# Optimization experiments

Hardware: AMD Instinct MI355X
Metric: run time of the kernel (lower is better)

Reference implementation:

```python
import jax, jax.numpy as jnp
import numpy as np

B, S, D, H = 2, 2048, 1024, 16
DH = D // H

def setup_inputs() -> dict:
    key = jax.random.key(0)
    ks = jax.random.split(key, 12)
    def lin(kw, kb, fan_in):
        bound = 1.0 / np.sqrt(fan_in)
        W = jax.random.uniform(kw, (D, D), jnp.float32, -bound, bound)
        b = jax.random.uniform(kb, (D,), jnp.float32, -bound, bound)
        return W, b
    Wq, bq = lin(ks[0], ks[1], D)
    Wk, bk = lin(ks[2], ks[3], D)
    Wv, bv = lin(ks[4], ks[5], D)
    Wo, bo = lin(ks[6], ks[7], D)
    q = jax.random.normal(ks[8], (B, S, D), jnp.float32)
    k = jax.random.normal(ks[9], (B, S, D), jnp.float32)
    v = jax.random.normal(ks[10], (B, S, D), jnp.float32)
    # causal mask (1 = keep, 0 = masked), broadcastable to [B,H,S,S]
    mask = jnp.tril(jnp.ones((S, S), jnp.int32))[None, None, :, :]
    return {"q": q, "k": k, "v": v, "mask": mask,
            "Wq": Wq, "bq": bq, "Wk": Wk, "bk": bk,
            "Wv": Wv, "bv": bv, "Wo": Wo, "bo": bo}

def reference(q, k, v, mask, Wq, bq, Wk, bk, Wv, bv, Wo, bo):
    # projections: torch Linear is x @ W.T + b
    def split(x):  # [B,S,D] -> [B,H,S,DH]
        return x.reshape(B, S, H, DH).transpose(0, 2, 1, 3)
    qh = split(q @ Wq.T + bq)
    kh = split(k @ Wk.T + bk)
    vh = split(v @ Wv.T + bv)
    score = jnp.einsum('bhqd,bhkd->bhqk', qh, kh) / jnp.sqrt(jnp.float32(DH))
    score = jnp.where(mask == 0, jnp.float32(-1e9), score)
    attn = jax.nn.softmax(score, axis=-1)
    out = jnp.einsum('bhqk,bhkd->bhqd', attn, vh)
    out = out.transpose(0, 2, 1, 3).reshape(B, S, D)
    return out @ Wo.T + bo, attn
```

## Files before the change

### kernel.cpp

```cpp
#include <hip/hip_runtime.h>

#define S_LEN 2048
#define D_MODEL 1024
#define N_HEADS 16
#define D_HEAD 64
#define BATCH 2

typedef __bf16 bf16;
typedef __bf16 bf16x8 __attribute__((ext_vector_type(8)));
typedef __bf16 bf16x4 __attribute__((ext_vector_type(4)));
typedef float f32x4 __attribute__((ext_vector_type(4)));

__device__ __forceinline__ f32x4 mfma16(bf16x8 a, bf16x8 b, f32x4 c) {
  return __builtin_amdgcn_mfma_f32_16x16x32_bf16(a, b, c, 0, 0, 0);
}

__device__ __forceinline__ void gload16(const bf16* g, bf16* lds) {
  __builtin_amdgcn_global_load_lds((const __attribute__((address_space(1))) void*)g,
                                   (__attribute__((address_space(3))) void*)lds, 16, 0, 0);
}

__global__ __launch_bounds__(256) void cvt_w(
    const float* __restrict__ s0, const float* __restrict__ s1,
    const float* __restrict__ s2, const float* __restrict__ s3,
    bf16* __restrict__ d0, bf16* __restrict__ d1, bf16* __restrict__ d2,
    bf16* __restrict__ d3) {
  const int y = blockIdx.y;
  const float* s = (y == 0) ? s0 : (y == 1) ? s1 : (y == 2) ? s2 : s3;
  bf16* d = (y == 0) ? d0 : (y == 1) ? d1 : (y == 2) ? d2 : d3;
  const int i = blockIdx.x * blockDim.x + threadIdx.x;
  const f32x4 a = *(const f32x4*)(s + (size_t)i * 8);
  const f32x4 b = *(const f32x4*)(s + (size_t)i * 8 + 4);
  bf16x8 o;
  o[0] = (bf16)a[0]; o[1] = (bf16)a[1]; o[2] = (bf16)a[2]; o[3] = (bf16)a[3];
  o[4] = (bf16)b[0]; o[5] = (bf16)b[1]; o[6] = (bf16)b[2]; o[7] = (bf16)b[3];
  *(bf16x8*)(d + (size_t)i * 8) = o;
}

__device__ __forceinline__ void gemm_loop(const bf16* __restrict__ gA,
                                          const bf16* __restrict__ gB,
                                          bf16* As, bf16* Bs,
                                          f32x4 (&acc)[4][4], int tid) {
  const int l = tid & 63;
  const int w = tid >> 6;
  const int wr = w >> 1, wc = w & 1;
  const int lr = l & 15, lg = l >> 4;
  const int lrow8 = l >> 3;
  const int colg = ((l & 7) ^ (lrow8 & 7)) * 8;

  for (int k0 = 0; k0 < D_MODEL; k0 += 64) {
#pragma unroll
    for (int i = 0; i < 4; ++i) {
      const int c = w * 4 + i;
      const int row = c * 8 + lrow8;
      gload16(gA + (size_t)row * D_MODEL + k0 + colg, As + c * 512);
      gload16(gB + (size_t)row * D_MODEL + k0 + colg, Bs + c * 512);
    }
    __syncthreads();
#pragma unroll
    for (int half = 0; half < 2; ++half) {
      bf16x8 af[4], bfb[4];
#pragma unroll
      for (int mm = 0; mm < 4; ++mm) {
        const int row = wr * 64 + mm * 16 + lr;
        af[mm] = *(const bf16x8*)(As + row * 64 + ((half * 4 + lg) ^ (lr & 7)) * 8);
      }
#pragma unroll
      for (int nn = 0; nn < 4; ++nn) {
        const int row = wc * 64 + nn * 16 + lr;
        bfb[nn] = *(const bf16x8*)(Bs + row * 64 + ((half * 4 + lg) ^ (lr & 7)) * 8);
      }
#pragma unroll
      for (int mm = 0; mm < 4; ++mm)
#pragma unroll
        for (int nn = 0; nn < 4; ++nn)
          acc[mm][nn] = mfma16(af[mm], bfb[nn], acc[mm][nn]);
    }
    __syncthreads();
  }
}

__device__ __forceinline__ void gemm_loop_af32(const float* __restrict__ gA32,
                                               const bf16* __restrict__ gB,
                                               bf16* As, bf16* Bs,
                                               f32x4 (&acc)[4][4], int tid) {
  const int l = tid & 63;
  const int w = tid >> 6;
  const int wr = w >> 1, wc = w & 1;
  const int lr = l & 15, lg = l >> 4;
  const int lrow8 = l >> 3;
  const int colg = ((l & 7) ^ (lrow8 & 7)) * 8;

  const int arow = tid >> 1;
  const int ahalf = tid & 1;
  const float* aptr = gA32 + (size_t)arow * D_MODEL + ahalf * 32;
  bf16* awr = As + arow * 64;

  for (int k0 = 0; k0 < D_MODEL; k0 += 64) {
    f32x4 av[8];
#pragma unroll
    for (int c = 0; c < 8; ++c) av[c] = *(const f32x4*)(aptr + k0 + c * 4);
#pragma unroll
    for (int i = 0; i < 4; ++i) {
      const int c = w * 4 + i;
      const int row = c * 8 + lrow8;
      gload16(gB + (size_t)row * D_MODEL + k0 + colg, Bs + c * 512);
    }
#pragma unroll
    for (int c8 = 0; c8 < 4; ++c8) {
      bf16x8 o;
#pragma unroll
      for (int e = 0; e < 4; ++e) {
        o[e] = (bf16)av[c8 * 2][e];
        o[e + 4] = (bf16)av[c8 * 2 + 1][e];
      }
      const int col16 = ahalf * 4 + c8;
      *(bf16x8*)(awr + (col16 ^ (arow & 7)) * 8) = o;
    }
    __syncthreads();
#pragma unroll
    for (int half = 0; half < 2; ++half) {
      bf16x8 af[4], bfb[4];
#pragma unroll
      for (int mm = 0; mm < 4; ++mm) {
        const int row = wr * 64 + mm * 16 + lr;
        af[mm] = *(const bf16x8*)(As + row * 64 + ((half * 4 + lg) ^ (lr & 7)) * 8);
      }
#pragma unroll
      for (int nn = 0; nn < 4; ++nn) {
        const int row = wc * 64 + nn * 16 + lr;
        bfb[nn] = *(const bf16x8*)(Bs + row * 64 + ((half * 4 + lg) ^ (lr & 7)) * 8);
      }
#pragma unroll
      for (int mm = 0; mm < 4; ++mm)
#pragma unroll
        for (int nn = 0; nn < 4; ++nn)
          acc[mm][nn] = mfma16(af[mm], bfb[nn], acc[mm][nn]);
    }
    __syncthreads();
  }
}

__global__ __launch_bounds__(256) void gemm_qkv(
    const float* __restrict__ qf, const float* __restrict__ kf,
    const float* __restrict__ vf, const bf16* __restrict__ Wqb,
    const bf16* __restrict__ Wkb, const bf16* __restrict__ Wvb,
    const float* __restrict__ biasq, const float* __restrict__ biask,
    const float* __restrict__ biasv, bf16* __restrict__ qhw,
    bf16* __restrict__ khw, bf16* __restrict__ vtw) {
  __shared__ bf16 As[128 * 64];
  __shared__ bf16 Bs[128 * 64];
  __shared__ bf16 T[128][72];
  const int z = blockIdx.z;
  const float* A = (z == 0) ? qf : (z == 1) ? kf : vf;
  const bf16* W = (z == 0) ? Wqb : (z == 1) ? Wkb : Wvb;
  const float* bias = (z == 0) ? biasq : (z == 1) ? biask : biasv;
  const float scale = (z == 0) ? 0.125f : 1.0f;
  bf16* out = (z == 0) ? qhw : (z == 1) ? khw : vtw;

  const int tid = threadIdx.x;
  const int l = tid & 63;
  const int w = tid >> 6;
  const int wr = w >> 1, wc = w & 1;
  const int lr = l & 15, lg = l >> 4;

  f32x4 acc[4][4] = {};
  gemm_loop_af32(A + ((size_t)blockIdx.x * 128) * D_MODEL,
                 W + ((size_t)blockIdx.y * 128) * D_MODEL, As, Bs, acc, tid);

  const int b = (blockIdx.x * 128) >> 11;
  const int s0 = (blockIdx.x * 128) & 2047;

  if (z == 2) {
#pragma unroll
    for (int half = 0; half < 2; ++half) {
      if (wc == half) {
#pragma unroll
        for (int nn = 0; nn < 4; ++nn) {
          const int n = blockIdx.y * 128 + half * 64 + nn * 16 + lr;
          const float bv = bias[n];
#pragma unroll
          for (int mm = 0; mm < 4; ++mm)
#pragma unroll
            for (int r = 0; r < 4; ++r) {
              const int ml = wr * 64 + mm * 16 + lg * 4 + r;
              T[ml][nn * 16 + lr] = (bf16)(acc[mm][nn][r] + bv);
            }
        }
      }
      __syncthreads();
      const int d = tid & 63;
      const int sblk = (tid >> 6) * 32;
      const int hglob = blockIdx.y * 2 + half;
      bf16* orow = vtw + (((size_t)(b * N_HEADS + hglob)) * D_HEAD + d) * S_LEN + s0 + sblk;
#pragma unroll
      for (int j = 0; j < 4; ++j) {
        bf16x8 pk;
#pragma unroll
        for (int e = 0; e < 8; ++e) pk[e] = T[sblk + j * 8 + e][d];
        *(bf16x8*)(orow + j * 8) = pk;
      }
      __syncthreads();
    }
  } else {
#pragma unroll
    for (int half = 0; half < 2; ++half) {
      if (wc == half) {
#pragma unroll
        for (int nn = 0; nn < 4; ++nn) {
          const int n = blockIdx.y * 128 + half * 64 + nn * 16 + lr;
          const float bv = bias[n];
#pragma unroll
          for (int mm = 0; mm < 4; ++mm)
#pragma unroll
            for (int r = 0; r < 4; ++r) {
              const int ml = wr * 64 + mm * 16 + lg * 4 + r;
              T[ml][nn * 16 + lr] = (bf16)((acc[mm][nn][r] + bv) * scale);
            }
        }
      }
      __syncthreads();
      const int hglob = blockIdx.y * 2 + half;
      bf16* obase = out + ((size_t)(b * N_HEADS + hglob) * S_LEN + s0) * D_HEAD;
      const int rsub = tid >> 3;
      const int d8 = (tid & 7) * 8;
#pragma unroll
      for (int j = 0; j < 4; ++j) {
        const int row_l = j * 32 + rsub;
        *(bf16x8*)(obase + (size_t)row_l * D_HEAD + d8) = *(const bf16x8*)(&T[row_l][d8]);
      }
      __syncthreads();
    }
  }
}

__device__ __forceinline__ void stage_strip(const bf16* __restrict__ src,
                                            size_t rstride, bf16* lds, int tid) {
#pragma unroll
  for (int rnd = 0; rnd < 2; ++rnd) {
    const int chunk = rnd * 256 + tid;
    const int row = chunk >> 3;
    const int c8 = chunk & 7;
    const int src8 = c8 ^ (row & 7);
    gload16(src + (size_t)row * rstride + src8 * 8, lds + chunk * 8);
  }
}

__global__ __launch_bounds__(256) void attn_flash(const bf16* __restrict__ qh,
                                                  const bf16* __restrict__ kh,
                                                  const bf16* __restrict__ vt,
                                                  bf16* __restrict__ ctx,
                                                  float* __restrict__ lbuf) {
  __shared__ bf16 Kb[2][64 * 64];
  __shared__ bf16 Vb[2][64 * 64];
  __shared__ bf16 P[4][16][72];
  const int tid = threadIdx.x;
  const int w = tid >> 6, l = tid & 63;
  const int lr = l & 15, lg = l >> 4;
  const int bh = blockIdx.y;
  const int bxx = blockIdx.x;
  const int qgroup = (bxx & 1) ? (31 - (bxx >> 1)) : (bxx >> 1);
  const int q0 = qgroup * 64 + w * 16;
  const int qrow = q0 + lr;
  const bf16* qp = qh + (size_t)bh * S_LEN * D_HEAD;
  const bf16* kp = kh + (size_t)bh * S_LEN * D_HEAD;
  const bf16* vp = vt + (size_t)bh * D_HEAD * S_LEN;

  const bf16x8 qf0 = *(const bf16x8*)(qp + (size_t)qrow * D_HEAD + lg * 8);
  const bf16x8 qf1 = *(const bf16x8*)(qp + (size_t)qrow * D_HEAD + 32 + lg * 8);

  const float NINF = -__builtin_inff();
  const int nfull = qgroup;
  const int x0 = (lg ^ (lr & 7)) * 8;
  const int x1 = ((4 | lg) ^ (lr & 7)) * 8;

  stage_strip(kp, D_HEAD, Kb[0], tid);
  stage_strip(vp, S_LEN, Vb[0], tid);
  __syncthreads();

  float lsum = 0.f;
  f32x4 oacc[4] = {};
  int cur = 0;

  for (int st = 0; st < nfull; ++st) {
    stage_strip(kp + (size_t)(st + 1) * 64 * D_HEAD, D_HEAD, Kb[cur ^ 1], tid);
    stage_strip(vp + (st + 1) * 64, S_LEN, Vb[cur ^ 1], tid);

    float ps = 0.f;
    __builtin_amdgcn_s_setprio(1);
    f32x4 zz4[4];
#pragma unroll
    for (int t = 0; t < 4; ++t) {
      const bf16* krow = Kb[cur] + (t * 16 + lr) * 64;
      f32x4 zz = {};
      zz = mfma16(*(const bf16x8*)(krow + x0), qf0, zz);
      zz = mfma16(*(const bf16x8*)(krow + x1), qf1, zz);
      zz4[t] = zz;
    }
    __builtin_amdgcn_s_setprio(0);
#pragma unroll
    for (int t = 0; t < 4; ++t) {
      bf16x4 pk;
#pragma unroll
      for (int r = 0; r < 4; ++r) {
        const float e = __expf(fminf(zz4[t][r], 60.f));
        ps += e;
        pk[r] = (bf16)e;
      }
      *(bf16x4*)(&P[w][lr][t * 16 + lg * 4]) = pk;
    }
    ps += __shfl_xor(ps, 16);
    ps += __shfl_xor(ps, 32);
    lsum += ps;
    const bf16x8 pb0 = *(const bf16x8*)(&P[w][lr][lg * 8]);
    const bf16x8 pb1 = *(const bf16x8*)(&P[w][lr][32 + lg * 8]);
    __builtin_amdgcn_s_setprio(1);
#pragma unroll
    for (int dt = 0; dt < 4; ++dt) {
      const bf16* vrow = Vb[cur] + (dt * 16 + lr) * 64;
      oacc[dt] = mfma16(*(const bf16x8*)(vrow + x0), pb0, oacc[dt]);
      oacc[dt] = mfma16(*(const bf16x8*)(vrow + x1), pb1, oacc[dt]);
    }
    __builtin_amdgcn_s_setprio(0);
    __syncthreads();
    cur ^= 1;
  }

  {
    float ps = 0.f;
#pragma unroll
    for (int t = 0; t < 4; ++t) {
      bf16x4 pk;
      if (t <= w) {
        const bf16* krow = Kb[cur] + (t * 16 + lr) * 64;
        f32x4 zz = {};
        zz = mfma16(*(const bf16x8*)(krow + x0), qf0, zz);
        zz = mfma16(*(const bf16x8*)(krow + x1), qf1, zz);
#pragma unroll
        for (int r = 0; r < 4; ++r) {
          const float sv = (t == w && (lg * 4 + r) > lr) ? NINF : zz[r];
          const float e = __expf(fminf(sv, 60.f));
          ps += e;
          pk[r] = (bf16)e;
        }
      } else {
#pragma unroll
        for (int r = 0; r < 4; ++r) pk[r] = (bf16)0.f;
      }
      *(bf16x4*)(&P[w][lr][t * 16 + lg * 4]) = pk;
    }
    ps += __shfl_xor(ps, 16);
    ps += __shfl_xor(ps, 32);
    lsum += ps;
    const bf16x8 pb0 = *(const bf16x8*)(&P[w][lr][lg * 8]);
    const bf16x8 pb1 = *(const bf16x8*)(&P[w][lr][32 + lg * 8]);
#pragma unroll
    for (int dt = 0; dt < 4; ++dt) {
      const bf16* vrow = Vb[cur] + (dt * 16 + lr) * 64;
      oacc[dt] = mfma16(*(const bf16x8*)(vrow + x0), pb0, oacc[dt]);
      oacc[dt] = mfma16(*(const bf16x8*)(vrow + x1), pb1, oacc[dt]);
    }
  }

  const float invl = 1.0f / lsum;
  const int b = bh >> 4, h = bh & 15;
  bf16* crow = ctx + ((size_t)(b * S_LEN + qrow)) * D_MODEL + h * D_HEAD;
#pragma unroll
  for (int dt = 0; dt < 4; ++dt) {
    bf16x4 ov;
#pragma unroll
    for (int r = 0; r < 4; ++r) ov[r] = (bf16)(oacc[dt][r] * invl);
    *(bf16x4*)(crow + dt * 16 + lg * 4) = ov;
  }
  if (lg == 0) lbuf[(size_t)bh * S_LEN + qrow] = invl;
}

__global__ __launch_bounds__(256) void mat_out(
    const bf16* __restrict__ qh, const bf16* __restrict__ kh,
    const float* __restrict__ lbuf, float* __restrict__ attn,
    const bf16* __restrict__ ctxA, const bf16* __restrict__ Wo,
    const float* __restrict__ bo, float* __restrict__ outp) {
  __shared__ __align__(16) char smem[34048];
  const int bid = blockIdx.x;
  const int tid = threadIdx.x;
  const int w = tid >> 6, l = tid & 63;
  const int lr = l & 15, lg = l >> 4;

  if (bid < 256) {
    bf16* As = (bf16*)smem;
    bf16* Bs = (bf16*)(smem + 16384);
    const int bx = bid & 31, by = bid >> 5;
    const int wr = w >> 1, wc = w & 1;
    f32x4 acc[4][4] = {};
    gemm_loop(ctxA + ((size_t)bx * 128) * D_MODEL,
              Wo + ((size_t)by * 128) * D_MODEL, As, Bs, acc, tid);
    const int rowg0 = bx * 128 + wr * 64;
    const int colg0 = by * 128 + wc * 64;
#pragma unroll
    for (int nn = 0; nn < 4; ++nn) {
      const int n = colg0 + nn * 16 + lr;
      const float bv = bo[n];
#pragma unroll
      for (int mm = 0; mm < 4; ++mm)
#pragma unroll
        for (int r = 0; r < 4; ++r) {
          const int m = rowg0 + mm * 16 + lg * 4 + r;
          __builtin_nontemporal_store(acc[mm][nn][r] + bv,
                                      outp + (size_t)m * D_MODEL + n);
        }
    }
    return;
  }

  bf16* Pt = (bf16*)smem;
  const int mid = bid - 256;
  const int q0 = (mid & 31) * 64;
  const int k0b = ((mid >> 5) & 7) * 256;
  const int bh = mid >> 8;
  float* ap = attn + (size_t)bh * S_LEN * S_LEN;

  if (k0b > q0 + 63) {
    const f32x4 zv = {};
#pragma unroll
    for (int j = 0; j < 4; ++j) {
      const int q = q0 + w * 16 + j * 4 + lg;
      float* rp = ap + (size_t)q * S_LEN + k0b + lr * 4;
#pragma unroll
      for (int sub = 0; sub < 4; ++sub)
        __builtin_nontemporal_store(zv, (f32x4*)(rp + sub * 64));
    }
    return;
  }

  const int k0 = k0b + w * 64;
  if (k0 <= q0 + 63) {
    const bf16* qp = qh + (size_t)bh * S_LEN * D_HEAD;
    const bf16* kp = kh + (size_t)bh * S_LEN * D_HEAD;
    float iv[4];
#pragma unroll
    for (int qs = 0; qs < 4; ++qs)
      iv[qs] = lbuf[(size_t)bh * S_LEN + q0 + qs * 16 + lr];
    bf16x8 kf[4][2], qf[4][2];
#pragma unroll
    for (int kt = 0; kt < 4; ++kt) {
      kf[kt][0] = *(const bf16x8*)(kp + (size_t)(k0 + kt * 16 + lr) * D_HEAD + lg * 8);
      kf[kt][1] = *(const bf16x8*)(kp + (size_t)(k0 + kt * 16 + lr) * D_HEAD + 32 + lg * 8);
    }
#pragma unroll
    for (int qs = 0; qs < 4; ++qs) {
      qf[qs][0] = *(const bf16x8*)(qp + (size_t)(q0 + qs * 16 + lr) * D_HEAD + lg * 8);
      qf[qs][1] = *(const bf16x8*)(qp + (size_t)(q0 + qs * 16 + lr) * D_HEAD + 32 + lg * 8);
    }
    f32x4 acc[4][4] = {};
#pragma unroll
    for (int qs = 0; qs < 4; ++qs)
#pragma unroll
      for (int kt = 0; kt < 4; ++kt) {
        acc[qs][kt] = mfma16(kf[kt][0], qf[qs][0], acc[qs][kt]);
        acc[qs][kt] = mfma16(kf[kt][1], qf[qs][1], acc[qs][kt]);
      }
#pragma unroll
    for (int qs = 0; qs < 4; ++qs) {
      const int q = q0 + qs * 16 + lr;
#pragma unroll
      for (int kt = 0; kt < 4; ++kt) {
        const int kbase = k0 + kt * 16 + lg * 4;
        bf16x4 pk;
#pragma unroll
        for (int r = 0; r < 4; ++r) {
          const float pv = (kbase + r > q)
                               ? 0.f
                               : __expf(fminf(acc[qs][kt][r], 60.f)) * iv[qs];
          pk[r] = (bf16)pv;
        }
        *(bf16x4*)(Pt + (qs * 16 + lr) * 264 + w * 64 + kt * 16 + lg * 4) = pk;
      }
    }
  } else {
    const bf16x4 z4 = {};
#pragma unroll
    for (int j = 0; j < 16; ++j)
      *(bf16x4*)(Pt + (j * 4 + lg) * 264 + w * 64 + lr * 4) = z4;
  }
  __syncthreads();

#pragma unroll
  for (int j = 0; j < 4; ++j) {
    const int rowl = w * 16 + j * 4 + lg;
    float* rp = ap + (size_t)(q0 + rowl) * S_LEN + k0b + lr * 4;
#pragma unroll
    for (int sub = 0; sub < 4; ++sub) {
      const bf16x4 pk = *(const bf16x4*)(Pt + rowl * 264 + sub * 64 + lr * 4);
      f32x4 o;
      o[0] = (float)pk[0]; o[1] = (float)pk[1];
      o[2] = (float)pk[2]; o[3] = (float)pk[3];
      __builtin_nontemporal_store(o, (f32x4*)(rp + sub * 64));
    }
  }
}

extern "C" void kernel_launch(void* const* d_in, const int* in_sizes, int n_in,
                              void* d_out, int out_size, void* d_ws, size_t ws_size,
                              hipStream_t stream) {
  (void)in_sizes; (void)n_in; (void)out_size; (void)ws_size;
  const float* q  = (const float*)d_in[0];
  const float* k  = (const float*)d_in[1];
  const float* v  = (const float*)d_in[2];
  const float* Wq = (const float*)d_in[4];
  const float* bq = (const float*)d_in[5];
  const float* Wk = (const float*)d_in[6];
  const float* bk = (const float*)d_in[7];
  const float* Wv = (const float*)d_in[8];
  const float* bv = (const float*)d_in[9];
  const float* Wo = (const float*)d_in[10];
  const float* bo = (const float*)d_in[11];

  float* outp = (float*)d_out;
  float* attn = outp + (size_t)BATCH * S_LEN * D_MODEL;

  char* ws = (char*)d_ws;
  bf16* qhw  = (bf16*)(ws);
  bf16* khw  = (bf16*)(ws + (8u << 20));
  bf16* vtw  = (bf16*)(ws + (16u << 20));
  bf16* ctxb = (bf16*)(ws + (24u << 20));
  bf16* Wqb  = (bf16*)(ws + (32u << 20));
  bf16* Wkb  = (bf16*)(ws + (34u << 20));
  bf16* Wvb  = (bf16*)(ws + (36u << 20));
  bf16* Wob  = (bf16*)(ws + (38u << 20));
  float* lbuf = (float*)(ws + (40u << 20));

  dim3 bb(256);
  cvt_w<<<dim3(512, 4), bb, 0, stream>>>(Wq, Wk, Wv, Wo, Wqb, Wkb, Wvb, Wob);
  gemm_qkv<<<dim3(32, 8, 3), bb, 0, stream>>>(q, k, v, Wqb, Wkb, Wvb,
                                              bq, bk, bv, qhw, khw, vtw);
  attn_flash<<<dim3(32, 32), bb, 0, stream>>>(qhw, khw, vtw, ctxb, lbuf);
  mat_out<<<dim3(8448), bb, 0, stream>>>(qhw, khw, lbuf, attn,
                                         ctxb, Wob, bo, outp);
}
```

Measured before the change: 277.0 us.

## Widen attention q-tile to 128 rows and move masked-zero attn stores into flash kernel

Each attention wave now processes two 16-row query fragments, so every K/V fragment read from LDS feeds twice as many MFMAs. Blocks cover 128 query rows, and the diagonal tile is handled inside the main loop per wave. Zero-filling of the fully masked upper-triangle attention blocks moves from mat_out into extra blocks of attn_flash, so the zero stores overlap with flash compute. mat_out then launches only the lower-triangular tiles, indexed through a triangular decode. This adds register pressure and some causal load imbalance across waves.

Result: slower. 286.7 us (+3.5%).

```diff
diff --git a/kernel.cpp b/kernel.cpp
--- a/kernel.cpp
+++ b/kernel.cpp
@@ -246,133 +246,184 @@
   }
 }
 
-__global__ __launch_bounds__(256) void attn_flash(const bf16* __restrict__ qh,
-                                                  const bf16* __restrict__ kh,
-                                                  const bf16* __restrict__ vt,
-                                                  bf16* __restrict__ ctx,
-                                                  float* __restrict__ lbuf) {
-  __shared__ bf16 Kb[2][64 * 64];
-  __shared__ bf16 Vb[2][64 * 64];
-  __shared__ bf16 P[4][16][72];
+__global__ __launch_bounds__(256) void attn_flash(
+    const bf16* __restrict__ qh, const bf16* __restrict__ kh,
+    const bf16* __restrict__ vt, bf16* __restrict__ ctx,
+    float* __restrict__ lbuf, float* __restrict__ attn) {
+  __shared__ bf16 Kb[2][4096];
+  __shared__ bf16 Vb[2][4096];
+  __shared__ bf16 P[4][2][16][72];
   const int tid = threadIdx.x;
   const int w = tid >> 6, l = tid & 63;
   const int lr = l & 15, lg = l >> 4;
-  const int bh = blockIdx.y;
-  const int bxx = blockIdx.x;
-  const int qgroup = (bxx & 1) ? (31 - (bxx >> 1)) : (bxx >> 1);
-  const int q0 = qgroup * 64 + w * 16;
-  const int qrow = q0 + lr;
+  const int bx = blockIdx.x, bh = blockIdx.y;
+
+  if (bx >= 16) {
+    int rem = bx - 16, zq = 0, cnt = 7;
+    while (rem >= cnt) { rem -= cnt; --cnt; ++zq; }
+    const int kq = zq + 1 + rem;
+    float* base = attn + (size_t)bh * S_LEN * S_LEN + (size_t)(zq * 256) * S_LEN + kq * 256;
+    const f32x4 zv = {};
+    for (int it = 0; it < 64; ++it) {
+      float* rp = base + (size_t)(it * 4 + w) * S_LEN + l * 4;
+      __builtin_nontemporal_store(zv, (f32x4*)rp);
+    }
+    return;
+  }
+
+  const int qg = (bx & 1) ? (15 - (bx >> 1)) : (bx >> 1);
+  const int q0w = qg * 128 + w * 32;
   const bf16* qp = qh + (size_t)bh * S_LEN * D_HEAD;
   const bf16* kp = kh + (size_t)bh * S_LEN * D_HEAD;
   const bf16* vp = vt + (size_t)bh * D_HEAD * S_LEN;
 
-  const bf16x8 qf0 = *(const bf16x8*)(qp + (size_t)qrow * D_HEAD + lg * 8);
-  const bf16x8 qf1 = *(const bf16x8*)(qp + (size_t)qrow * D_HEAD + 32 + lg * 8);
+  bf16x8 qf[2][2];
+#pragma unroll
+  for (int f = 0; f < 2; ++f) {
+    qf[f][0] = *(const bf16x8*)(qp + (size_t)(q0w + f * 16 + lr) * D_HEAD + lg * 8);
+    qf[f][1] = *(const bf16x8*)(qp + (size_t)(q0w + f * 16 + lr) * D_HEAD + 32 + lg * 8);
+  }
 
   const float NINF = -__builtin_inff();
-  const int nfull = qgroup;
   const int x0 = (lg ^ (lr & 7)) * 8;
   const int x1 = ((4 | lg) ^ (lr & 7)) * 8;
+  const int nfull = 2 * qg + (w >> 1);
+  const int smax = 2 * qg + 1;
 
   stage_strip(kp, D_HEAD, Kb[0], tid);
   stage_strip(vp, S_LEN, Vb[0], tid);
   __syncthreads();
 
-  float lsum = 0.f;
-  f32x4 oacc[4] = {};
+  float lsum[2] = {0.f, 0.f};
+  f32x4 oacc[2][4] = {};
   int cur = 0;
 
-  for (int st = 0; st < nfull; ++st) {
-    stage_strip(kp + (size_t)(st + 1) * 64 * D_HEAD, D_HEAD, Kb[cur ^ 1], tid);
-    stage_strip(vp + (st + 1) * 64, S_LEN, Vb[cur ^ 1], tid);
-
-    float ps = 0.f;
-    __builtin_amdgcn_s_setprio(1);
-    f32x4 zz4[4];
-#pragma unroll
-    for (int t = 0; t < 4; ++t) {
-      const bf16* krow = Kb[cur] + (t * 16 + lr) * 64;
-      f32x4 zz = {};
-      zz = mfma16(*(const bf16x8*)(krow + x0), qf0, zz);
-      zz = mfma16(*(const bf16x8*)(krow + x1), qf1, zz);
-      zz4[t] = zz;
-    }
-    __builtin_amdgcn_s_setprio(0);
-#pragma unroll
-    for (int t = 0; t < 4; ++t) {
-      bf16x4 pk;
-#pragma unroll
-      for (int r = 0; r < 4; ++r) {
-        const float e = __expf(fminf(zz4[t][r], 60.f));
-        ps += e;
-        pk[r] = (bf16)e;
-      }
-      *(bf16x4*)(&P[w][lr][t * 16 + lg * 4]) = pk;
-    }
-    ps += __shfl_xor(ps, 16);
-    ps += __shfl_xor(ps, 32);
-    lsum += ps;
-    const bf16x8 pb0 = *(const bf16x8*)(&P[w][lr][lg * 8]);
-    const bf16x8 pb1 = *(const bf16x8*)(&P[w][lr][32 + lg * 8]);
-    __builtin_amdgcn_s_setprio(1);
-#pragma unroll
-    for (int dt = 0; dt < 4; ++dt) {
-      const bf16* vrow = Vb[cur] + (dt * 16 + lr) * 64;
-      oacc[dt] = mfma16(*(const bf16x8*)(vrow + x0), pb0, oacc[dt]);
-      oacc[dt] = mfma16(*(const bf16x8*)(vrow + x1), pb1, oacc[dt]);
-    }
-    __builtin_amdgcn_s_setprio(0);
+  for (int st = 0; st <= smax; ++st) {
+    if (st < smax) {
+      stage_strip(kp + (size_t)(st + 1) * 64 * D_HEAD, D_HEAD, Kb[cur ^ 1], tid);
+      stage_strip(vp + (st + 1) * 64, S_LEN, Vb[cur ^ 1], tid);
+    }
+    if (st < nfull) {
+      f32x4 zz[2][4];
+      __builtin_amdgcn_s_setprio(1);
+#pragma unroll
+      for (int t = 0; t < 4; ++t) {
+        const bf16* krow = Kb[cur] + (t * 16 + lr) * 64;
+        const bf16x8 a0 = *(const bf16x8*)(krow + x0);
+        const bf16x8 a1 = *(const bf16x8*)(krow + x1);
+#pragma unroll
+        for (int f = 0; f < 2; ++f) {
+          f32x4 z = {};
+          z = mfma16(a0, qf[f][0], z);
+          z = mfma16(a1, qf[f][1], z);
+          zz[f][t] = z;
+        }
+      }
+      __builtin_amdgcn_s_setprio(0);
+#pragma unroll
+      for (int f = 0; f < 2; ++f) {
+        float ps = 0.f;
+#pragma unroll
+        for (int t = 0; t < 4; ++t) {
+          bf16x4 pk;
+#pragma unroll
+          for (int r = 0; r < 4; ++r) {
+            const float e = __expf(fminf(zz[f][t][r], 60.f));
+            ps += e;
+            pk[r] = (bf16)e;
+          }
+          *(bf16x4*)(&P[w][f][lr][t * 16 + lg * 4]) = pk;
+        }
+        ps += __shfl_xor(ps, 16);
+        ps += __shfl_xor(ps, 32);
+        lsum[f] += ps;
+      }
+      bf16x8 pb[2][2];
+#pragma unroll
+      for (int f = 0; f < 2; ++f) {
+        pb[f][0] = *(const bf16x8*)(&P[w][f][lr][lg * 8]);
+        pb[f][1] = *(const bf16x8*)(&P[w][f][lr][32 + lg * 8]);
+      }
+      __builtin_amdgcn_s_setprio(1);
+#pragma unroll
+      for (int dt = 0; dt < 4; ++dt) {
+        const bf16* vrow = Vb[cur] + (dt * 16 + lr) * 64;
+        const bf16x8 v0 = *(const bf16x8*)(vrow + x0);
+        const bf16x8 v1 = *(const bf16x8*)(vrow + x1);
+#pragma unroll
+        for (int f = 0; f < 2; ++f) {
+          oacc[f][dt] = mfma16(v0, pb[f][0], oacc[f][dt]);
+          oacc[f][dt] = mfma16(v1, pb[f][1], oacc[f][dt]);
+        }
+      }
+      __builtin_amdgcn_s_setprio(0);
+    } else if (st == nfull) {
+#pragma unroll
+      for (int f = 0; f < 2; ++f) {
+        const int tdiag = (2 * w + f) & 3;
+        float ps = 0.f;
+#pragma unroll
+        for (int t = 0; t < 4; ++t) {
+          bf16x4 pk;
+          if (t <= tdiag) {
+            const bf16* krow = Kb[cur] + (t * 16 + lr) * 64;
+            f32x4 z = {};
+            z = mfma16(*(const bf16x8*)(krow + x0), qf[f][0], z);
+            z = mfma16(*(const bf16x8*)(krow + x1), qf[f][1], z);
+#pragma unroll
+            for (int r = 0; r < 4; ++r) {
+              const float sv = (t == tdiag && (lg * 4 + r) > lr) ? NINF : z[r];
+              const float e = __expf(fminf(sv, 60.f));
+              ps += e;
+              pk[r] = (bf16)e;
+            }
+          } else {
+#pragma unroll
+            for (int r = 0; r < 4; ++r) pk[r] = (bf16)0.f;
+          }
+          *(bf16x4*)(&P[w][f][lr][t * 16 + lg * 4]) = pk;
+        }
+        ps += __shfl_xor(ps, 16);
+        ps += __shfl_xor(ps, 32);
+        lsum[f] += ps;
+      }
+      bf16x8 pb[2][2];
+#pragma unroll
+      for (int f = 0; f < 2; ++f) {
+        pb[f][0] = *(const bf16x8*)(&P[w][f][lr][lg * 8]);
+        pb[f][1] = *(const bf16x8*)(&P[w][f][lr][32 + lg * 8]);
+      }
+#pragma unroll
+      for (int dt = 0; dt < 4; ++dt) {
+        const bf16* vrow = Vb[cur] + (dt * 16 + lr) * 64;
+        const bf16x8 v0 = *(const bf16x8*)(vrow + x0);
+        const bf16x8 v1 = *(const bf16x8*)(vrow + x1);
+#pragma unroll
+        for (int f = 0; f < 2; ++f) {
+          oacc[f][dt] = mfma16(v0, pb[f][0], oacc[f][dt]);
+          oacc[f][dt] = mfma16(v1, pb[f][1], oacc[f][dt]);
+        }
+      }
+    }
     __syncthreads();
     cur ^= 1;
   }
 
-  {
-    float ps = 0.f;
-#pragma unroll
-    for (int t = 0; t < 4; ++t) {
-      bf16x4 pk;
-      if (t <= w) {
-        const bf16* krow = Kb[cur] + (t * 16 + lr) * 64;
-        f32x4 zz = {};
-        zz = mfma16(*(const bf16x8*)(krow + x0), qf0, zz);
-        zz = mfma16(*(const bf16x8*)(krow + x1), qf1, zz);
-#pragma unroll
-        for (int r = 0; r < 4; ++r) {
-          const float sv = (t == w && (lg * 4 + r) > lr) ? NINF : zz[r];
-          const float e = __expf(fminf(sv, 60.f));
-          ps += e;
-          pk[r] = (bf16)e;
-        }
-      } else {
-#pragma unroll
-        for (int r = 0; r < 4; ++r) pk[r] = (bf16)0.f;
-      }
-      *(bf16x4*)(&P[w][lr][t * 16 + lg * 4]) = pk;
-    }
-    ps += __shfl_xor(ps, 16);
-    ps += __shfl_xor(ps, 32);
-    lsum += ps;
-    const bf16x8 pb0 = *(const bf16x8*)(&P[w][lr][lg * 8]);
-    const bf16x8 pb1 = *(const bf16x8*)(&P[w][lr][32 + lg * 8]);
+  const int b = bh >> 4, h = bh & 15;
+#pragma unroll
+  for (int f = 0; f < 2; ++f) {
+    const float invl = 1.0f / lsum[f];
+    const int qrow = q0w + f * 16 + lr;
+    bf16* crow = ctx + ((size_t)(b * S_LEN + qrow)) * D_MODEL + h * D_HEAD;
 #pragma unroll
     for (int dt = 0; dt < 4; ++dt) {
-      const bf16* vrow = Vb[cur] + (dt * 16 + lr) * 64;
-      oacc[dt] = mfma16(*(const bf16x8*)(vrow + x0), pb0, oacc[dt]);
-      oacc[dt] = mfma16(*(const bf16x8*)(vrow + x1), pb1, oacc[dt]);
-    }
-  }
-
-  const float invl = 1.0f / lsum;
-  const int b = bh >> 4, h = bh & 15;
-  bf16* crow = ctx + ((size_t)(b * S_LEN + qrow)) * D_MODEL + h * D_HEAD;
-#pragma unroll
-  for (int dt = 0; dt < 4; ++dt) {
-    bf16x4 ov;
-#pragma unroll
-    for (int r = 0; r < 4; ++r) ov[r] = (bf16)(oacc[dt][r] * invl);
-    *(bf16x4*)(crow + dt * 16 + lg * 4) = ov;
-  }
-  if (lg == 0) lbuf[(size_t)bh * S_LEN + qrow] = invl;
+      bf16x4 ov;
+#pragma unroll
+      for (int r = 0; r < 4; ++r) ov[r] = (bf16)(oacc[f][dt][r] * invl);
+      *(bf16x4*)(crow + dt * 16 + lg * 4) = ov;
+    }
+    if (lg == 0) lbuf[(size_t)bh * S_LEN + qrow] = invl;
+  }
 }
 
 __global__ __launch_bounds__(256) void mat_out(
@@ -414,23 +465,16 @@
 
   bf16* Pt = (bf16*)smem;
   const int mid = bid - 256;
-  const int q0 = (mid & 31) * 64;
-  const int k0b = ((mid >> 5) & 7) * 256;
-  const int bh = mid >> 8;
+  const int bh = mid / 144;
+  int rem = mid - bh * 144;
+  int g = 0;
+  while (2 * (g + 1) * (g + 2) <= rem) ++g;
+  const int rem2 = rem - 2 * g * (g + 1);
+  const int q0t = 4 * g + rem2 / (g + 1);
+  const int kq = rem2 - (g + 1) * (rem2 / (g + 1));
+  const int q0 = q0t * 64;
+  const int k0b = kq * 256;
   float* ap = attn + (size_t)bh * S_LEN * S_LEN;
-
-  if (k0b > q0 + 63) {
-    const f32x4 zv = {};
-#pragma unroll
-    for (int j = 0; j < 4; ++j) {
-      const int q = q0 + w * 16 + j * 4 + lg;
-      float* rp = ap + (size_t)q * S_LEN + k0b + lr * 4;
-#pragma unroll
-      for (int sub = 0; sub < 4; ++sub)
-        __builtin_nontemporal_store(zv, (f32x4*)(rp + sub * 64));
-    }
-    return;
-  }
 
   const int k0 = k0b + w * 64;
   if (k0 <= q0 + 63) {
@@ -533,7 +577,7 @@
   cvt_w<<<dim3(512, 4), bb, 0, stream>>>(Wq, Wk, Wv, Wo, Wqb, Wkb, Wvb, Wob);
   gemm_qkv<<<dim3(32, 8, 3), bb, 0, stream>>>(q, k, v, Wqb, Wkb, Wvb,
                                               bq, bk, bv, qhw, khw, vtw);
-  attn_flash<<<dim3(32, 32), bb, 0, stream>>>(qhw, khw, vtw, ctxb, lbuf);
-  mat_out<<<dim3(8448), bb, 0, stream>>>(qhw, khw, lbuf, attn,
-                                         ctxb, Wob, bo, outp);
-}
+  attn_flash<<<dim3(44, 32), bb, 0, stream>>>(qhw, khw, vtw, ctxb, lbuf, attn);
+  mat_out<<<dim3(256 + 4608), bb, 0, stream>>>(qhw, khw, lbuf, attn,
+                                               ctxb, Wob, bo, outp);
+}
```

## Move causal zero-fill of attention matrix into flash kernel extra blocks

Applied to the files above, without the earlier changes.

Zeroing of the fully masked upper-triangular 256x256 tiles of the attention-probability output moves out of mat_out and into 28 extra blocks per head in attn_flash. mat_out is launched only over the lower-triangular tiles, using a triangular index decode. The idea is to let the zero stores overlap with the latency-bound flash attention and to shrink the mat_out grid. The cost is more scalar index arithmetic in both kernels and extra write traffic while attention runs.

Measured after the change: 266.4 us. 3.8% less time.

```diff
diff --git a/kernel.cpp b/kernel.cpp
--- a/kernel.cpp
+++ b/kernel.cpp
@@ -246,11 +246,10 @@
   }
 }
 
-__global__ __launch_bounds__(256) void attn_flash(const bf16* __restrict__ qh,
-                                                  const bf16* __restrict__ kh,
-                                                  const bf16* __restrict__ vt,
-                                                  bf16* __restrict__ ctx,
-                                                  float* __restrict__ lbuf) {
+__global__ __launch_bounds__(256) void attn_flash(
+    const bf16* __restrict__ qh, const bf16* __restrict__ kh,
+    const bf16* __restrict__ vt, bf16* __restrict__ ctx,
+    float* __restrict__ lbuf, float* __restrict__ attn) {
   __shared__ bf16 Kb[2][64 * 64];
   __shared__ bf16 Vb[2][64 * 64];
   __shared__ bf16 P[4][16][72];
@@ -259,6 +258,20 @@
   const int lr = l & 15, lg = l >> 4;
   const int bh = blockIdx.y;
   const int bxx = blockIdx.x;
+
+  if (bxx >= 32) {
+    int rem = bxx - 32, zq = 0, cnt = 7;
+    while (rem >= cnt) { rem -= cnt; --cnt; ++zq; }
+    const int kq = zq + 1 + rem;
+    float* base = attn + (size_t)bh * S_LEN * S_LEN + (size_t)(zq * 256) * S_LEN + kq * 256;
+    const f32x4 zv = {};
+    for (int it = 0; it < 64; ++it) {
+      float* rp = base + (size_t)(it * 4 + w) * S_LEN + l * 4;
+      __builtin_nontemporal_store(zv, (f32x4*)rp);
+    }
+    return;
+  }
+
   const int qgroup = (bxx & 1) ? (31 - (bxx >> 1)) : (bxx >> 1);
   const int q0 = qgroup * 64 + w * 16;
   const int qrow = q0 + lr;
@@ -414,23 +427,16 @@
 
   bf16* Pt = (bf16*)smem;
   const int mid = bid - 256;
-  const int q0 = (mid & 31) * 64;
-  const int k0b = ((mid >> 5) & 7) * 256;
-  const int bh = mid >> 8;
+  const int bh = mid / 144;
+  int rem = mid - bh * 144;
+  int g = 0;
+  while (2 * (g + 1) * (g + 2) <= rem) ++g;
+  const int rem2 = rem - 2 * g * (g + 1);
+  const int q0t = 4 * g + rem2 / (g + 1);
+  const int kq = rem2 - (g + 1) * (rem2 / (g + 1));
+  const int q0 = q0t * 64;
+  const int k0b = kq * 256;
   float* ap = attn + (size_t)bh * S_LEN * S_LEN;
-
-  if (k0b > q0 + 63) {
-    const f32x4 zv = {};
-#pragma unroll
-    for (int j = 0; j < 4; ++j) {
-      const int q = q0 + w * 16 + j * 4 + lg;
-      float* rp = ap + (size_t)q * S_LEN + k0b + lr * 4;
-#pragma unroll
-      for (int sub = 0; sub < 4; ++sub)
-        __builtin_nontemporal_store(zv, (f32x4*)(rp + sub * 64));
-    }
-    return;
-  }
 
   const int k0 = k0b + w * 64;
   if (k0 <= q0 + 63) {
@@ -533,7 +539,7 @@
   cvt_w<<<dim3(512, 4), bb, 0, stream>>>(Wq, Wk, Wv, Wo, Wqb, Wkb, Wvb, Wob);
   gemm_qkv<<<dim3(32, 8, 3), bb, 0, stream>>>(q, k, v, Wqb, Wkb, Wvb,
                                               bq, bk, bv, qhw, khw, vtw);
-  attn_flash<<<dim3(32, 32), bb, 0, stream>>>(qhw, khw, vtw, ctxb, lbuf);
-  mat_out<<<dim3(8448), bb, 0, stream>>>(qhw, khw, lbuf, attn,
-                                         ctxb, Wob, bo, outp);
-}
+  attn_flash<<<dim3(60, 32), bb, 0, stream>>>(qhw, khw, vtw, ctxb, lbuf, attn);
+  mat_out<<<dim3(256 + 4608), bb, 0, stream>>>(qhw, khw, lbuf, attn,
+                                               ctxb, Wob, bo, outp);
+}
```
